# Optimization experiments

Measured on AMD Instinct MI355X. Metric: run time of the kernel, lower is better.

## Reference

```python
import jax, jax.numpy as jnp
import numpy as np

B, D, O, I = 64, 128, 512, 512


def setup_inputs() -> dict:
    key = jax.random.key(0)
    k1, k2, k3 = jax.random.split(key, 3)
    inp = jax.random.bernoulli(k1, 0.5, (B, D, I))            # binary activations
    weight_noise = jax.random.bernoulli(k2, 0.5, (D, O, I))   # sigmoid(W) > rand, binary
    # popcount of I fair coins has mean I/2, std sqrt(I)/2; center threshold there
    bias_noise = (I / 2.0 + (jnp.sqrt(I) / 2.0)
                  * jax.random.normal(k3, (D, O), dtype=jnp.float32))
    return {"input": inp, "weight_noise": weight_noise, "bias_noise": bias_noise}


def reference(input, weight_noise, bias_noise):
    # (weight_noise == input).sum(-1) over binary {0,1} tensors equals
    #   dot(w, x) + dot(1-w, 1-x) = I - sum(w) - sum(x) + 2 * dot(w, x)
    # which avoids materializing the (B, D, O, I) comparison tensor.
    x = input.astype(jnp.float32)          # (B, D, I)
    w = weight_noise.astype(jnp.float32)   # (D, O, I)
    dot = jnp.einsum('bdi,doi->bdo', x, w)               # per-direction binary GEMM
    act = (jnp.float32(I) - w.sum(-1)[None, :, :]        # (1, D, O)
           - x.sum(-1)[:, :, None]                        # (B, D, 1)
           + 2.0 * dot)                                   # match counts, (B, D, O)
    return act > bias_noise[None, :, :]                   # bool (B, D, O)
```

## Files before the change

### kernel.cpp

```cpp
#include <hip/hip_runtime.h>
#include <cstdint>

typedef unsigned long long u64;
typedef unsigned int u32;

#define BB 64
#define DD 128
#define OO 512
#define II 512
#define OT 64

__device__ __forceinline__ int detect_mode(const u32* __restrict__ w) {
    bool all01 = true, allf = true;
#pragma unroll
    for (int i = 0; i < 32; ++i) {
        u32 v = w[i];
        all01 = all01 && (v <= 1u);
        allf  = allf  && (v == 0u || v == 0x3F800000u);
    }
    return all01 ? 1 : (allf ? 2 : 0);
}

__device__ __forceinline__ u64 pack_row(const void* __restrict__ src,
                                        size_t elem0, int mode, int lane) {
    u64 my = 0;
    if (mode == 0) {
        u64 v = *(const u64*)((const uint8_t*)src + elem0 + (size_t)lane * 8);
#pragma unroll
        for (int j = 0; j < 8; ++j) {
            u64 bj = __ballot(((u32)(v >> (8 * j))) & 1u);
            if (lane == j) my = bj;
        }
    } else {
        const u32 sh = (mode == 1) ? 0u : 23u;
        const uint4* p = (const uint4*)((const u32*)src + elem0);
        uint4 v0 = p[lane];
        uint4 v1 = p[64 + lane];
        u32 b0 = (v0.x >> sh) & 1u, b1 = (v0.y >> sh) & 1u;
        u32 b2 = (v0.z >> sh) & 1u, b3 = (v0.w >> sh) & 1u;
        u32 b4 = (v1.x >> sh) & 1u, b5 = (v1.y >> sh) & 1u;
        u32 b6 = (v1.z >> sh) & 1u, b7 = (v1.w >> sh) & 1u;
        u64 w0 = __ballot(b0), w1 = __ballot(b1), w2 = __ballot(b2), w3 = __ballot(b3);
        u64 w4 = __ballot(b4), w5 = __ballot(b5), w6 = __ballot(b6), w7 = __ballot(b7);
        if (lane == 0) my = w0;  if (lane == 1) my = w1;
        if (lane == 2) my = w2;  if (lane == 3) my = w3;
        if (lane == 4) my = w4;  if (lane == 5) my = w5;
        if (lane == 6) my = w6;  if (lane == 7) my = w7;
    }
    return my;
}

__global__ __launch_bounds__(256)
void binlin_one(const void* __restrict__ x, const void* __restrict__ w,
                const float* __restrict__ bias, int* __restrict__ out) {
    __shared__ u64 wp[OT][9];
    __shared__ u64 xp[BB][8];

    const int tid  = threadIdx.x;
    const int bid  = blockIdx.x;
    const int xcd = bid & 7;
    const int idx = bid >> 3;
    const int d   = xcd * 16 + (idx >> 3);
    const int o0  = (idx & 7) * OT;
    const int wv   = tid >> 6;
    const int lane = tid & 63;

    const int mode = detect_mode((const u32*)w);

#pragma unroll
    for (int r = 0; r < 16; ++r) {
        const int o = wv * 16 + r;
        u64 my = pack_row(w, ((size_t)(d * OO + o0 + o)) * II, mode, lane);
        if (lane < 8) wp[o][lane] = my;
    }
#pragma unroll
    for (int r = 0; r < 16; ++r) {
        const int b = wv * 16 + r;
        u64 my = pack_row(x, ((size_t)(b * DD + d)) * II, mode, lane);
        if (lane < 8) xp[b][lane] = my;
    }
    const float bv = bias[d * OO + o0 + (tid & 63)];
    __syncthreads();

    const int o  = tid & 63;
    const int b0 = (tid >> 6) * 16;

    u64 wr[8];
#pragma unroll
    for (int k = 0; k < 8; ++k) wr[k] = wp[o][k];

    int* outp = out + (size_t)d * OO + o0 + o;
#pragma unroll 4
    for (int bi = 0; bi < 16; ++bi) {
        const int b = b0 + bi;
        int m = 0;
#pragma unroll
        for (int k = 0; k < 8; ++k) m += __popcll(xp[b][k] ^ wr[k]);
        const float act = (float)(512 - m);
        outp[(size_t)b * (DD * OO)] = (act > bv) ? 1 : 0;
    }
}

extern "C" void kernel_launch(void* const* d_in, const int* in_sizes, int n_in,
                              void* d_out, int out_size, void* d_ws, size_t ws_size,
                              hipStream_t stream) {
    const void*  x    = d_in[0];
    const void*  w    = d_in[1];
    const float* bias = (const float*)d_in[2];
    int*         out  = (int*)d_out;

    binlin_one<<<DD * (OO / OT), 256, 0, stream>>>(x, w, bias, out);
}
```

Measured before the change: 38.55 us.

## Prepack activations in separate kernel and pack weights per-thread without ballots

Moves bit-packing of x into a separate pre-pass kernel that writes 32-bit packed words to workspace. Before, every (d, o-tile) block re-packed the x rows, so each x row was packed 8 times. The main kernel now packs weights with per-thread contiguous loads and shift-or arithmetic instead of wave ballots, and uses a padded u32 LDS layout with 32-bit popcounts. This adds a second launch and a workspace round trip in exchange for removing the redundant x reads and the ballot overhead.

```diff
diff --git a/kernel.cpp b/kernel.cpp
--- a/kernel.cpp
+++ b/kernel.cpp
@@ -9,6 +9,9 @@
 #define OO 512
 #define II 512
 #define OT 64
+#define WPR 16
+#define XROWS (BB * DD)
+#define LROW 17
 
 __device__ __forceinline__ int detect_mode(const u32* __restrict__ w) {
     bool all01 = true, allf = true;
@@ -21,63 +24,82 @@
     return all01 ? 1 : (allf ? 2 : 0);
 }
 
-__device__ __forceinline__ u64 pack_row(const void* __restrict__ src,
-                                        size_t elem0, int mode, int lane) {
-    u64 my = 0;
-    if (mode == 0) {
-        u64 v = *(const u64*)((const uint8_t*)src + elem0 + (size_t)lane * 8);
+__device__ __forceinline__ u32 nib4(u32 v) {
+    return (v | (v >> 7) | (v >> 14) | (v >> 21)) & 0xFu;
+}
+__device__ __forceinline__ u32 pack32_bytes(uint4 a, uint4 b) {
+    return  nib4(a.x)        | (nib4(a.y) << 4)  | (nib4(a.z) << 8)  |
+           (nib4(a.w) << 12) | (nib4(b.x) << 16) | (nib4(b.y) << 20) |
+           (nib4(b.z) << 24) | (nib4(b.w) << 28);
+}
+__device__ __forceinline__ u32 pack32_words(const u32* __restrict__ p, u32 sh) {
+    u32 r = 0;
 #pragma unroll
-        for (int j = 0; j < 8; ++j) {
-            u64 bj = __ballot(((u32)(v >> (8 * j))) & 1u);
-            if (lane == j) my = bj;
-        }
-    } else {
-        const u32 sh = (mode == 1) ? 0u : 23u;
-        const uint4* p = (const uint4*)((const u32*)src + elem0);
-        uint4 v0 = p[lane];
-        uint4 v1 = p[64 + lane];
-        u32 b0 = (v0.x >> sh) & 1u, b1 = (v0.y >> sh) & 1u;
-        u32 b2 = (v0.z >> sh) & 1u, b3 = (v0.w >> sh) & 1u;
-        u32 b4 = (v1.x >> sh) & 1u, b5 = (v1.y >> sh) & 1u;
-        u32 b6 = (v1.z >> sh) & 1u, b7 = (v1.w >> sh) & 1u;
-        u64 w0 = __ballot(b0), w1 = __ballot(b1), w2 = __ballot(b2), w3 = __ballot(b3);
-        u64 w4 = __ballot(b4), w5 = __ballot(b5), w6 = __ballot(b6), w7 = __ballot(b7);
-        if (lane == 0) my = w0;  if (lane == 1) my = w1;
-        if (lane == 2) my = w2;  if (lane == 3) my = w3;
-        if (lane == 4) my = w4;  if (lane == 5) my = w5;
-        if (lane == 6) my = w6;  if (lane == 7) my = w7;
+    for (int i = 0; i < 32; i += 4) {
+        uint4 v = *(const uint4*)(p + i);
+        r |= (((v.x >> sh) & 1u) << i)       | (((v.y >> sh) & 1u) << (i + 1)) |
+             (((v.z >> sh) & 1u) << (i + 2)) | (((v.w >> sh) & 1u) << (i + 3));
     }
-    return my;
+    return r;
 }
 
 __global__ __launch_bounds__(256)
-void binlin_one(const void* __restrict__ x, const void* __restrict__ w,
-                const float* __restrict__ bias, int* __restrict__ out) {
-    __shared__ u64 wp[OT][9];
-    __shared__ u64 xp[BB][8];
+void pack_x_kernel(const void* __restrict__ x, const void* __restrict__ w,
+                   u32* __restrict__ px) {
+    const int t = blockIdx.x * 256 + threadIdx.x;
+    const int mode = detect_mode((const u32*)w);
+    u32 word;
+    if (mode == 0) {
+        const uint8_t* p = (const uint8_t*)x + (size_t)t * 32;
+        uint4 a = *(const uint4*)p, b = *(const uint4*)(p + 16);
+        word = pack32_bytes(a, b);
+    } else {
+        word = pack32_words((const u32*)x + (size_t)t * 32, mode == 1 ? 0u : 23u);
+    }
+    px[t] = word;
+}
 
-    const int tid  = threadIdx.x;
-    const int bid  = blockIdx.x;
+__global__ __launch_bounds__(256, 4)
+void fused_kernel(const void* __restrict__ w, const u32* __restrict__ px,
+                  const float* __restrict__ bias, int* __restrict__ out) {
+    __shared__ u32 wpl[OT * LROW];
+    __shared__ u32 xpl[BB * LROW];
+
+    const int tid = threadIdx.x;
+    const int bid = blockIdx.x;
     const int xcd = bid & 7;
     const int idx = bid >> 3;
     const int d   = xcd * 16 + (idx >> 3);
     const int o0  = (idx & 7) * OT;
-    const int wv   = tid >> 6;
-    const int lane = tid & 63;
 
     const int mode = detect_mode((const u32*)w);
 
+    if (mode == 0) {
+        const uint8_t* tb = (const uint8_t*)w + (size_t)(d * OO + o0) * II
+                          + (size_t)tid * 128;
+        uint4 va[8];
 #pragma unroll
-    for (int r = 0; r < 16; ++r) {
-        const int o = wv * 16 + r;
-        u64 my = pack_row(w, ((size_t)(d * OO + o0 + o)) * II, mode, lane);
-        if (lane < 8) wp[o][lane] = my;
+        for (int i = 0; i < 8; ++i)
+            va[i] = *(const uint4*)(tb + 16 * i);
+#pragma unroll
+        for (int i = 0; i < 4; ++i) {
+            const int f = 4 * tid + i;
+            wpl[(f >> 4) * LROW + (f & 15)] = pack32_bytes(va[2 * i], va[2 * i + 1]);
+        }
+    } else {
+        const u32 sh = (mode == 1) ? 0u : 23u;
+        const u32* tb = (const u32*)w + (size_t)(d * OO + o0) * II + (size_t)tid * 128;
+#pragma unroll
+        for (int i = 0; i < 4; ++i) {
+            const int f = 4 * tid + i;
+            wpl[(f >> 4) * LROW + (f & 15)] = pack32_words(tb + 32 * i, sh);
+        }
     }
 #pragma unroll
-    for (int r = 0; r < 16; ++r) {
-        const int b = wv * 16 + r;
-        u64 my = pack_row(x, ((size_t)(b * DD + d)) * II, mode, lane);
-        if (lane < 8) xp[b][lane] = my;
+    for (int j = 0; j < 4; ++j) {
+        const int f = 256 * j + tid;
+        const int b = f >> 4, k = f & 15;
+        xpl[b * LROW + k] = px[((size_t)(b * DD + d) << 4) | k];
     }
     const float bv = bias[d * OO + o0 + (tid & 63)];
     __syncthreads();
@@ -85,9 +107,9 @@
     const int o  = tid & 63;
     const int b0 = (tid >> 6) * 16;
 
-    u64 wr[8];
+    u32 wr[WPR];
 #pragma unroll
-    for (int k = 0; k < 8; ++k) wr[k] = wp[o][k];
+    for (int k = 0; k < WPR; ++k) wr[k] = wpl[o * LROW + k];
 
     int* outp = out + (size_t)d * OO + o0 + o;
 #pragma unroll 4
@@ -95,7 +117,7 @@
         const int b = b0 + bi;
         int m = 0;
 #pragma unroll
-        for (int k = 0; k < 8; ++k) m += __popcll(xp[b][k] ^ wr[k]);
+        for (int k = 0; k < WPR; ++k) m += __popc(xpl[b * LROW + k] ^ wr[k]);
         const float act = (float)(512 - m);
         outp[(size_t)b * (DD * OO)] = (act > bv) ? 1 : 0;
     }
@@ -108,6 +130,8 @@
     const void*  w    = d_in[1];
     const float* bias = (const float*)d_in[2];
     int*         out  = (int*)d_out;
+    u32*         px   = (u32*)d_ws;
 
-    binlin_one<<<DD * (OO / OT), 256, 0, stream>>>(x, w, bias, out);
+    pack_x_kernel<<<XROWS * WPR / 256, 256, 0, stream>>>(x, w, px);
+    fused_kernel<<<DD * (OO / OT), 256, 0, stream>>>(w, px, bias, out);
 }
```

After: 43.10 us. +11.8%, slower.

## Pack byte-bool rows with multiply bit-gather and batch all loads upfront

Applied to the files above, without the earlier changes.

For byte-encoded boolean inputs, each lane now packs its 8 bytes into one byte using a multiply-shift nibble gather and writes that byte to shared memory, replacing eight ballots per row. All 32 row loads per thread are issued before any packing so memory latency overlaps, and the bias load moves earlier. The packed x tile gets a padded row stride, and the launch bounds request 4 blocks per SM. The bit order changes to per-lane bytes, but it matches between x and w, so popcount results stay correct. The cost is extra registers for 32 outstanding u64 loads.

```diff
diff --git a/kernel.cpp b/kernel.cpp
--- a/kernel.cpp
+++ b/kernel.cpp
@@ -9,6 +9,7 @@
 #define OO 512
 #define II 512
 #define OT 64
+#define LROW 72
 
 __device__ __forceinline__ int detect_mode(const u32* __restrict__ w) {
     bool all01 = true, allf = true;
@@ -21,65 +22,85 @@
     return all01 ? 1 : (allf ? 2 : 0);
 }
 
-__device__ __forceinline__ u64 pack_row(const void* __restrict__ src,
-                                        size_t elem0, int mode, int lane) {
+__device__ __forceinline__ u32 nib4(u32 v) {
+    return ((v * 0x01020408u) >> 24) & 0xFu;
+}
+__device__ __forceinline__ u32 byte8(u64 v) {
+    return nib4((u32)v) | (nib4((u32)(v >> 32)) << 4);
+}
+
+__device__ __forceinline__ u64 pack_row_ballot(const void* __restrict__ src,
+                                               size_t elem0, int mode, int lane) {
+    const u32 sh = (mode == 1) ? 0u : 23u;
+    const uint4* p = (const uint4*)((const u32*)src + elem0);
+    uint4 a = p[lane];
+    uint4 b = p[64 + lane];
+    u64 w0 = __ballot((a.x >> sh) & 1u), w1 = __ballot((a.y >> sh) & 1u);
+    u64 w2 = __ballot((a.z >> sh) & 1u), w3 = __ballot((a.w >> sh) & 1u);
+    u64 w4 = __ballot((b.x >> sh) & 1u), w5 = __ballot((b.y >> sh) & 1u);
+    u64 w6 = __ballot((b.z >> sh) & 1u), w7 = __ballot((b.w >> sh) & 1u);
     u64 my = 0;
-    if (mode == 0) {
-        u64 v = *(const u64*)((const uint8_t*)src + elem0 + (size_t)lane * 8);
-#pragma unroll
-        for (int j = 0; j < 8; ++j) {
-            u64 bj = __ballot(((u32)(v >> (8 * j))) & 1u);
-            if (lane == j) my = bj;
-        }
-    } else {
-        const u32 sh = (mode == 1) ? 0u : 23u;
-        const uint4* p = (const uint4*)((const u32*)src + elem0);
-        uint4 v0 = p[lane];
-        uint4 v1 = p[64 + lane];
-        u32 b0 = (v0.x >> sh) & 1u, b1 = (v0.y >> sh) & 1u;
-        u32 b2 = (v0.z >> sh) & 1u, b3 = (v0.w >> sh) & 1u;
-        u32 b4 = (v1.x >> sh) & 1u, b5 = (v1.y >> sh) & 1u;
-        u32 b6 = (v1.z >> sh) & 1u, b7 = (v1.w >> sh) & 1u;
-        u64 w0 = __ballot(b0), w1 = __ballot(b1), w2 = __ballot(b2), w3 = __ballot(b3);
-        u64 w4 = __ballot(b4), w5 = __ballot(b5), w6 = __ballot(b6), w7 = __ballot(b7);
-        if (lane == 0) my = w0;  if (lane == 1) my = w1;
-        if (lane == 2) my = w2;  if (lane == 3) my = w3;
-        if (lane == 4) my = w4;  if (lane == 5) my = w5;
-        if (lane == 6) my = w6;  if (lane == 7) my = w7;
-    }
+    if (lane == 0) my = w0;  if (lane == 1) my = w1;
+    if (lane == 2) my = w2;  if (lane == 3) my = w3;
+    if (lane == 4) my = w4;  if (lane == 5) my = w5;
+    if (lane == 6) my = w6;  if (lane == 7) my = w7;
     return my;
 }
 
-__global__ __launch_bounds__(256)
+__global__ __launch_bounds__(256, 4)
 void binlin_one(const void* __restrict__ x, const void* __restrict__ w,
                 const float* __restrict__ bias, int* __restrict__ out) {
     __shared__ u64 wp[OT][9];
-    __shared__ u64 xp[BB][8];
+    __shared__ u64 xp[BB][9];
 
     const int tid  = threadIdx.x;
     const int bid  = blockIdx.x;
-    const int xcd = bid & 7;
-    const int idx = bid >> 3;
-    const int d   = xcd * 16 + (idx >> 3);
-    const int o0  = (idx & 7) * OT;
+    const int xcd  = bid & 7;
+    const int idx  = bid >> 3;
+    const int d    = xcd * 16 + (idx >> 3);
+    const int o0   = (idx & 7) * OT;
     const int wv   = tid >> 6;
     const int lane = tid & 63;
 
     const int mode = detect_mode((const u32*)w);
+    const float bv = bias[d * OO + o0 + (tid & 63)];
 
+    uint8_t* wpb = (uint8_t*)wp;
+    uint8_t* xpb = (uint8_t*)xp;
+
+    if (mode == 0) {
+        const uint8_t* wt = (const uint8_t*)w + (size_t)(d * OO + o0) * II;
+        const uint8_t* xb = (const uint8_t*)x;
+
+        u64 vw[16], vx[16];
 #pragma unroll
-    for (int r = 0; r < 16; ++r) {
-        const int o = wv * 16 + r;
-        u64 my = pack_row(w, ((size_t)(d * OO + o0 + o)) * II, mode, lane);
-        if (lane < 8) wp[o][lane] = my;
+        for (int r = 0; r < 16; ++r)
+            vw[r] = *(const u64*)(wt + (size_t)(wv * 16 + r) * II
+                                     + (size_t)lane * 8);
+#pragma unroll
+        for (int r = 0; r < 16; ++r)
+            vx[r] = *(const u64*)(xb + ((size_t)((wv * 16 + r) * DD + d)) * II
+                                     + (size_t)lane * 8);
+#pragma unroll
+        for (int r = 0; r < 16; ++r)
+            wpb[(wv * 16 + r) * LROW + lane] = (uint8_t)byte8(vw[r]);
+#pragma unroll
+        for (int r = 0; r < 16; ++r)
+            xpb[(wv * 16 + r) * LROW + lane] = (uint8_t)byte8(vx[r]);
+    } else {
+#pragma unroll
+        for (int r = 0; r < 16; ++r) {
+            const int o = wv * 16 + r;
+            u64 my = pack_row_ballot(w, ((size_t)(d * OO + o0 + o)) * II, mode, lane);
+            if (lane < 8) wp[o][lane] = my;
+        }
+#pragma unroll
+        for (int r = 0; r < 16; ++r) {
+            const int b = wv * 16 + r;
+            u64 my = pack_row_ballot(x, ((size_t)(b * DD + d)) * II, mode, lane);
+            if (lane < 8) xp[b][lane] = my;
+        }
     }
-#pragma unroll
-    for (int r = 0; r < 16; ++r) {
-        const int b = wv * 16 + r;
-        u64 my = pack_row(x, ((size_t)(b * DD + d)) * II, mode, lane);
-        if (lane < 8) xp[b][lane] = my;
-    }
-    const float bv = bias[d * OO + o0 + (tid & 63)];
     __syncthreads();
 
     const int o  = tid & 63;
```

New measurement: 38.96 us. About the same (+1.1%).
